# Kernel optimization log

Measured on AMD Instinct MI355X. Metric: run time of the kernel, lower is better.

## Reference

```python
import jax, jax.numpy as jnp
import numpy as np

D_MODEL = 1024
N_HEADS = 16
HEAD_DIM = D_MODEL // N_HEADS


def setup_inputs() -> dict:
    key = jax.random.key(0)
    ks = jax.random.split(key, 9)
    s = 1.0 / np.sqrt(D_MODEL)
    inp = {"x": jax.random.normal(ks[0], (4, 2048, D_MODEL), dtype=jnp.float32)}
    for i, name in enumerate(["q", "k", "v", "o"]):
        inp[f"W{name}"] = jax.random.uniform(ks[1 + i], (D_MODEL, D_MODEL), dtype=jnp.float32, minval=-s, maxval=s)
        inp[f"b{name}"] = jax.random.uniform(ks[5 + i], (D_MODEL,), dtype=jnp.float32, minval=-s, maxval=s)
    return inp


def reference(x, Wq, Wk, Wv, Wo, bq, bk, bv, bo):
    B, S, D = x.shape
    # linear layers: y = x @ W^T + b (torch nn.Linear convention)
    def proj(W, b):
        y = jnp.einsum('bsd,ed->bse', x, W) + b
        return y.reshape(B, S, N_HEADS, HEAD_DIM).transpose(0, 2, 1, 3)  # [B,H,S,hd]
    q = proj(Wq, bq)
    k = proj(Wk, bk)
    v = proj(Wv, bv)
    score = jnp.einsum('bhqd,bhkd->bhqk', q, k) / np.sqrt(HEAD_DIM)  # [B,H,S,S]
    attns = jax.nn.softmax(score, axis=-1)
    out = jnp.einsum('bhqk,bhkd->bhqd', attns, v)  # [B,H,S,hd]
    out = out.transpose(0, 2, 1, 3).reshape(B, S, D)
    return jnp.einsum('bsd,ed->bse', out, Wo) + bo
```

## Files before the change

### kernel.cpp

```cpp
#include <hip/hip_runtime.h>
#include <hip/hip_bf16.h>
#include <stdint.h>


typedef __attribute__((ext_vector_type(8))) short bfx8;
typedef __attribute__((ext_vector_type(4))) float fx4;

#define MFMA_16x16x32(A, B, C) __builtin_amdgcn_mfma_f32_16x16x32_bf16(A, B, C, 0, 0, 0)

__device__ __forceinline__ unsigned short f2bf(float f) {
  union { float f; uint32_t u; } v; v.f = f;
  uint32_t r = v.u + 0x7fffu + ((v.u >> 16) & 1u);
  return (unsigned short)(r >> 16);
}
__device__ __forceinline__ unsigned short bf16u(float f) {
  union { __hip_bfloat16 h; unsigned short u; } cv;
  cv.h = __float2bfloat16(f);
  return cv.u;
}
__device__ __forceinline__ void async16(unsigned short* l, const unsigned short* g) {
  __builtin_amdgcn_global_load_lds((const __attribute__((address_space(1))) void*)g,
                                   (__attribute__((address_space(3))) void*)l,
                                   16, 0, 0);
}

__global__ __launch_bounds__(256) void convert_f32_bf16(
    const float* __restrict__ src, unsigned short* __restrict__ dst, int n4) {
  const int i = blockIdx.x * 256 + threadIdx.x;
  if (i >= n4) return;
  const float4 v = ((const float4*)src)[i];
  ushort4 o;
  o.x = f2bf(v.x); o.y = f2bf(v.y); o.z = f2bf(v.z); o.w = f2bf(v.w);
  ((ushort4*)dst)[i] = o;
}

__global__ __launch_bounds__(256) void convert3_f32_bf16(
    const float* __restrict__ s0, const float* __restrict__ s1,
    const float* __restrict__ s2,
    unsigned short* __restrict__ d0, unsigned short* __restrict__ d1,
    unsigned short* __restrict__ d2, int n4) {
  const int which = blockIdx.y;
  const float* src = (which == 0) ? s0 : ((which == 1) ? s1 : s2);
  unsigned short* dst = (which == 0) ? d0 : ((which == 1) ? d1 : d2);
  const int i = blockIdx.x * 256 + threadIdx.x;
  if (i >= n4) return;
  const float4 v = ((const float4*)src)[i];
  ushort4 o;
  o.x = f2bf(v.x); o.y = f2bf(v.y); o.z = f2bf(v.z); o.w = f2bf(v.w);
  ((ushort4*)dst)[i] = o;
}


__global__ __launch_bounds__(256) void gemm_qkv(
    const unsigned short* __restrict__ X,
    const unsigned short* __restrict__ Wq, const unsigned short* __restrict__ Wk,
    const unsigned short* __restrict__ Wv,
    const float* __restrict__ bq, const float* __restrict__ bk,
    const float* __restrict__ bv,
    unsigned short* __restrict__ outq, unsigned short* __restrict__ outk,
    unsigned short* __restrict__ outv) {
  __shared__ unsigned short ldsA[128 * 32];
  __shared__ unsigned short ldsB[128 * 32];
  const int tid = threadIdx.x;
  const int w = tid >> 6, lane = tid & 63, quad = lane >> 4, l15 = lane & 15;
  const int m0 = blockIdx.x * 128;
  const int which = blockIdx.y >> 3;
  const int n0 = (blockIdx.y & 7) * 128;
  const unsigned short* W = (which == 0) ? Wq : ((which == 1) ? Wk : Wv);
  const float* bias       = (which == 0) ? bq : ((which == 1) ? bk : bv);
  unsigned short* Y       = (which == 0) ? outq : ((which == 1) ? outk : outv);
  const int wm = (w >> 1) * 64, wn = (w & 1) * 64;
  const int srow = tid >> 2, scol = (tid & 3) * 8;
  fx4 acc[4][4] = {};
  for (int k0 = 0; k0 < 1024; k0 += 32) {
    __syncthreads();
    async16(&ldsA[srow * 32 + scol],        X + (size_t)(m0 + srow) * 1024 + k0 + scol);
    async16(&ldsA[(srow + 64) * 32 + scol], X + (size_t)(m0 + srow + 64) * 1024 + k0 + scol);
    async16(&ldsB[srow * 32 + scol],        W + (size_t)(n0 + srow) * 1024 + k0 + scol);
    async16(&ldsB[(srow + 64) * 32 + scol], W + (size_t)(n0 + srow + 64) * 1024 + k0 + scol);
    __syncthreads();
    bfx8 af[4], bfr[4];
#pragma unroll
    for (int i = 0; i < 4; i++) af[i]  = *(const bfx8*)&ldsA[(wm + i * 16 + l15) * 32 + quad * 8];
#pragma unroll
    for (int j = 0; j < 4; j++) bfr[j] = *(const bfx8*)&ldsB[(wn + j * 16 + l15) * 32 + quad * 8];
#pragma unroll
    for (int i = 0; i < 4; i++)
#pragma unroll
      for (int j = 0; j < 4; j++)
        acc[i][j] = MFMA_16x16x32(af[i], bfr[j], acc[i][j]);
  }
  const float qscale = 0.18033688011112042f;
  float bv_[4];
#pragma unroll
  for (int j = 0; j < 4; j++) bv_[j] = bias[n0 + wn + j * 16 + l15];
#pragma unroll
  for (int i = 0; i < 4; i++) {
#pragma unroll
    for (int r = 0; r < 4; r++) {
      const int m_g = m0 + wm + i * 16 + quad * 4 + r;
      const int bb = m_g >> 11, ss = m_g & 2047;
#pragma unroll
      for (int j = 0; j < 4; j++) {
        const int n_g = n0 + wn + j * 16 + l15;
        const int h = n_g >> 6, d = n_g & 63;
        float o = acc[i][j][r] + bv_[j];
        if (which == 0) o *= qscale;
        if (which == 2)
          Y[((size_t)(bb * 16 + h) * 64 + d) * 2048 + ss] = f2bf(o);
        else
          Y[(((size_t)(bb * 16 + h)) * 2048 + ss) * 64 + d] = f2bf(o);
      }
    }
  }
}

__global__ __launch_bounds__(256) void gemm_o(
    const unsigned short* __restrict__ X,
    const unsigned short* __restrict__ W,
    const float* __restrict__ bias,
    float* __restrict__ Y) {
  __shared__ unsigned short ldsA[128 * 32];
  __shared__ unsigned short ldsB[128 * 32];
  const int tid = threadIdx.x;
  const int w = tid >> 6, lane = tid & 63, quad = lane >> 4, l15 = lane & 15;
  const int m0 = blockIdx.x * 128;
  const int n0 = blockIdx.y * 128;
  const int wm = (w >> 1) * 64, wn = (w & 1) * 64;
  const int srow = tid >> 2, scol = (tid & 3) * 8;
  fx4 acc[4][4] = {};
  for (int k0 = 0; k0 < 1024; k0 += 32) {
    __syncthreads();
    async16(&ldsA[srow * 32 + scol],        X + (size_t)(m0 + srow) * 1024 + k0 + scol);
    async16(&ldsA[(srow + 64) * 32 + scol], X + (size_t)(m0 + srow + 64) * 1024 + k0 + scol);
    async16(&ldsB[srow * 32 + scol],        W + (size_t)(n0 + srow) * 1024 + k0 + scol);
    async16(&ldsB[(srow + 64) * 32 + scol], W + (size_t)(n0 + srow + 64) * 1024 + k0 + scol);
    __syncthreads();
    bfx8 af[4], bfr[4];
#pragma unroll
    for (int i = 0; i < 4; i++) af[i]  = *(const bfx8*)&ldsA[(wm + i * 16 + l15) * 32 + quad * 8];
#pragma unroll
    for (int j = 0; j < 4; j++) bfr[j] = *(const bfx8*)&ldsB[(wn + j * 16 + l15) * 32 + quad * 8];
#pragma unroll
    for (int i = 0; i < 4; i++)
#pragma unroll
      for (int j = 0; j < 4; j++)
        acc[i][j] = MFMA_16x16x32(af[i], bfr[j], acc[i][j]);
  }
  float bv_[4];
#pragma unroll
  for (int j = 0; j < 4; j++) bv_[j] = bias[n0 + wn + j * 16 + l15];
#pragma unroll
  for (int i = 0; i < 4; i++) {
#pragma unroll
    for (int r = 0; r < 4; r++) {
      const int m_g = m0 + wm + i * 16 + quad * 4 + r;
#pragma unroll
      for (int j = 0; j < 4; j++) {
        const int n_g = n0 + wn + j * 16 + l15;
        Y[(size_t)m_g * 1024 + n_g] = acc[i][j][r] + bv_[j];
      }
    }
  }
}


#define P_LD 68

__global__ __launch_bounds__(256, 4) void attn_kernel(
    const unsigned short* __restrict__ Q, const unsigned short* __restrict__ K,
    const unsigned short* __restrict__ VT, unsigned short* __restrict__ O) {
  __shared__ unsigned short lds_k[64 * 64];
  __shared__ unsigned short lds_vt[64 * 64];
  __shared__ unsigned short lds_p[4][32 * P_LD];
  const int tid = threadIdx.x;
  const int w = tid >> 6, lane = tid & 63, quad = lane >> 4, l15 = lane & 15;
  const int bh = blockIdx.y;
  const size_t hoff = (size_t)bh * 2048 * 64;
  const unsigned short* Qh = Q + hoff;
  const unsigned short* Kh = K + hoff;
  const unsigned short* VTh = VT + hoff;
  const int q0 = blockIdx.x * 128 + w * 32;

  bfx8 qf[2][2];
#pragma unroll
  for (int s = 0; s < 2; s++) {
    qf[s][0] = *(const bfx8*)&Qh[(size_t)(q0 + s * 16 + l15) * 64 + quad * 8];
    qf[s][1] = *(const bfx8*)&Qh[(size_t)(q0 + s * 16 + l15) * 64 + 32 + quad * 8];
  }

  fx4 o_acc[2][4] = {};
  float l_r[2][4] = {};

  const int vr0 = w * 8 + (lane >> 3);
  const int vr1 = vr0 + 32;
  const int seg = lane & 7;
  const unsigned short* vsrc0 = VTh + (size_t)vr0 * 2048 + ((seg ^ (vr0 & 7)) * 8);
  const unsigned short* vsrc1 = VTh + (size_t)vr1 * 2048 + ((seg ^ (vr1 & 7)) * 8);
  unsigned short* vdst0 = &lds_vt[vr0 * 64 + seg * 8];
  unsigned short* vdst1 = &lds_vt[vr1 * 64 + seg * 8];

  const int krl = lane >> 3;
  unsigned short* kdst0 = &lds_k[(w * 16 + krl) * 64 + seg * 8];
  unsigned short* kdst1 = kdst0 + 8 * 64;
  const unsigned short* ksrc0 = Kh + (size_t)(w * 16 + krl) * 64 + ((seg ^ krl) * 8);
  const unsigned short* ksrc1 = ksrc0 + 8 * 64;

  const int s0v = (quad ^ (l15 & 7)) * 8;
  const int s1v = ((quad + 4) ^ (l15 & 7)) * 8;

  async16(kdst0, ksrc0);
  async16(kdst1, ksrc1);

  for (int t = 0; t < 32; ++t) {
    const int kv0 = t * 64;
    __syncthreads();
    async16(vdst0, vsrc0 + kv0);
    async16(vdst1, vsrc1 + kv0);

    fx4 s0a[4], s1a[4];
#pragma unroll
    for (int nj = 0; nj < 4; nj++) {
      const int krow = (nj * 16 + l15) * 64;
      bfx8 kf0 = *(const bfx8*)&lds_k[krow + s0v];
      bfx8 kf1 = *(const bfx8*)&lds_k[krow + s1v];
      fx4 z0 = {}, z1 = {};
      z0 = MFMA_16x16x32(qf[0][0], kf0, z0);
      z0 = MFMA_16x16x32(qf[0][1], kf1, z0);
      z1 = MFMA_16x16x32(qf[1][0], kf0, z1);
      z1 = MFMA_16x16x32(qf[1][1], kf1, z1);
      s0a[nj] = z0;
      s1a[nj] = z1;
    }

#pragma unroll
    for (int s = 0; s < 2; s++) {
      const fx4* sa = (s == 0) ? s0a : s1a;
#pragma unroll
      for (int r = 0; r < 4; r++) {
        float p0 = __builtin_amdgcn_exp2f(sa[0][r]);
        float p1 = __builtin_amdgcn_exp2f(sa[1][r]);
        float p2 = __builtin_amdgcn_exp2f(sa[2][r]);
        float p3 = __builtin_amdgcn_exp2f(sa[3][r]);
        l_r[s][r] += (p0 + p1) + (p2 + p3);
        const int pbase = (s * 16 + quad * 4 + r) * P_LD + l15;
        lds_p[w][pbase]      = bf16u(p0);
        lds_p[w][pbase + 16] = bf16u(p1);
        lds_p[w][pbase + 32] = bf16u(p2);
        lds_p[w][pbase + 48] = bf16u(p3);
      }
    }

    __syncthreads();

    bfx8 pf[2][2];
#pragma unroll
    for (int s = 0; s < 2; s++) {
      pf[s][0] = *(const bfx8*)&lds_p[w][(s * 16 + l15) * P_LD + quad * 8];
      pf[s][1] = *(const bfx8*)&lds_p[w][(s * 16 + l15) * P_LD + 32 + quad * 8];
    }
#pragma unroll
    for (int nj = 0; nj < 4; nj++) {
      const int vrow = (nj * 16 + l15) * 64;
      bfx8 vf0 = *(const bfx8*)&lds_vt[vrow + s0v];
      bfx8 vf1 = *(const bfx8*)&lds_vt[vrow + s1v];
      o_acc[0][nj] = MFMA_16x16x32(pf[0][0], vf0, o_acc[0][nj]);
      o_acc[0][nj] = MFMA_16x16x32(pf[0][1], vf1, o_acc[0][nj]);
      o_acc[1][nj] = MFMA_16x16x32(pf[1][0], vf0, o_acc[1][nj]);
      o_acc[1][nj] = MFMA_16x16x32(pf[1][1], vf1, o_acc[1][nj]);
    }

    if (t < 31) {
      const size_t koff = (size_t)(t + 1) * 64 * 64;
      async16(kdst0, ksrc0 + koff);
      async16(kdst1, ksrc1 + koff);
    }
  }

  const int bb = bh >> 4, h = bh & 15;
#pragma unroll
  for (int s = 0; s < 2; s++) {
#pragma unroll
    for (int r = 0; r < 4; r++) {
      float sum = l_r[s][r];
#pragma unroll
      for (int d = 1; d < 16; d <<= 1) sum += __shfl_xor(sum, d, 64);
      const float inv = 1.0f / sum;
      const int qrow = q0 + s * 16 + quad * 4 + r;
      const size_t base = ((size_t)(bb * 2048 + qrow)) * 1024 + h * 64;
#pragma unroll
      for (int nj = 0; nj < 4; nj++)
        O[base + nj * 16 + l15] = f2bf(o_acc[s][nj][r] * inv);
    }
  }
}


extern "C" void kernel_launch(void* const* d_in, const int* in_sizes, int n_in,
                              void* d_out, int out_size, void* d_ws, size_t ws_size,
                              hipStream_t stream) {
  const float* x = (const float*)d_in[0];
  const float *Wq, *Wk, *Wv, *Wo, *bq, *bk, *bv, *bo;
  if (in_sizes[2] == 1024) {
    Wq = (const float*)d_in[1]; bq = (const float*)d_in[2];
    Wk = (const float*)d_in[3]; bk = (const float*)d_in[4];
    Wv = (const float*)d_in[5]; bv = (const float*)d_in[6];
    Wo = (const float*)d_in[7]; bo = (const float*)d_in[8];
  } else {
    Wq = (const float*)d_in[1]; Wk = (const float*)d_in[2];
    Wv = (const float*)d_in[3]; Wo = (const float*)d_in[4];
    bq = (const float*)d_in[5]; bk = (const float*)d_in[6];
    bv = (const float*)d_in[7]; bo = (const float*)d_in[8];
  }
  const size_t NT = (size_t)4 * 16 * 2048 * 64;
  const size_t NW = (size_t)1024 * 1024;
  unsigned short* ws = (unsigned short*)d_ws;
  unsigned short* xb = ws;
  unsigned short* q  = ws + NT;
  unsigned short* k  = ws + 2 * NT;
  unsigned short* vt = ws + 3 * NT;
  unsigned short* ao = xb;
  unsigned short* wq = (unsigned short*)d_out;
  unsigned short* wk = wq + NW;
  unsigned short* wv = wk + NW;
  unsigned short* wo = q;

  convert_f32_bf16<<<(int)(NT / 4 + 255) / 256, 256, 0, stream>>>(x, xb, (int)(NT / 4));
  convert3_f32_bf16<<<dim3((int)(NW / 4 + 255) / 256, 3), 256, 0, stream>>>(
      Wq, Wk, Wv, wq, wk, wv, (int)(NW / 4));

  gemm_qkv<<<dim3(64, 24), 256, 0, stream>>>(xb, wq, wk, wv, bq, bk, bv, q, k, vt);
  attn_kernel<<<dim3(16, 64), 256, 0, stream>>>(q, k, vt, ao);

  convert_f32_bf16<<<(int)(NW / 4 + 255) / 256, 256, 0, stream>>>(Wo, wo, (int)(NW / 4));
  gemm_o<<<dim3(64, 8), 256, 0, stream>>>(ao, wo, bo, (float*)d_out);
}
```

Measured before the change: 298.3 us.

## Vectorize V-transpose stores and remap attention blocks to keep heads on one XCD

The QKV GEMM epilogue for the transposed V output now packs four consecutive sequence positions into one 8-byte ushort4 store, replacing four scattered 2-byte stores. The attention kernel switches to a 1D grid and decodes the block index so that all 16 query blocks of a given head land on the same XCD (blocks are dispatched round-robin across 8 XCDs). This lets that head's K/V tiles be reused from that XCD's L2. The remap assumes exactly 64 heads and 8 XCDs.

```diff
diff --git a/kernel.cpp b/kernel.cpp
--- a/kernel.cpp
+++ b/kernel.cpp
@@ -94,22 +94,38 @@
   float bv_[4];
 #pragma unroll
   for (int j = 0; j < 4; j++) bv_[j] = bias[n0 + wn + j * 16 + l15];
-#pragma unroll
-  for (int i = 0; i < 4; i++) {
-#pragma unroll
-    for (int r = 0; r < 4; r++) {
-      const int m_g = m0 + wm + i * 16 + quad * 4 + r;
+  if (which == 2) {
+#pragma unroll
+    for (int i = 0; i < 4; i++) {
+      const int m_g = m0 + wm + i * 16 + quad * 4;
       const int bb = m_g >> 11, ss = m_g & 2047;
 #pragma unroll
       for (int j = 0; j < 4; j++) {
         const int n_g = n0 + wn + j * 16 + l15;
         const int h = n_g >> 6, d = n_g & 63;
-        float o = acc[i][j][r] + bv_[j];
-        if (which == 0) o *= qscale;
-        if (which == 2)
-          Y[((size_t)(bb * 16 + h) * 64 + d) * 2048 + ss] = f2bf(o);
-        else
+        ushort4 o4;
+        o4.x = f2bf(acc[i][j][0] + bv_[j]);
+        o4.y = f2bf(acc[i][j][1] + bv_[j]);
+        o4.z = f2bf(acc[i][j][2] + bv_[j]);
+        o4.w = f2bf(acc[i][j][3] + bv_[j]);
+        *(ushort4*)&Y[((size_t)(bb * 16 + h) * 64 + d) * 2048 + ss] = o4;
+      }
+    }
+  } else {
+#pragma unroll
+    for (int i = 0; i < 4; i++) {
+#pragma unroll
+      for (int r = 0; r < 4; r++) {
+        const int m_g = m0 + wm + i * 16 + quad * 4 + r;
+        const int bb = m_g >> 11, ss = m_g & 2047;
+#pragma unroll
+        for (int j = 0; j < 4; j++) {
+          const int n_g = n0 + wn + j * 16 + l15;
+          const int h = n_g >> 6, d = n_g & 63;
+          float o = acc[i][j][r] + bv_[j];
+          if (which == 0) o *= qscale;
           Y[(((size_t)(bb * 16 + h)) * 2048 + ss) * 64 + d] = f2bf(o);
+        }
       }
     }
   }
@@ -175,12 +191,18 @@
   __shared__ unsigned short lds_p[4][32 * P_LD];
   const int tid = threadIdx.x;
   const int w = tid >> 6, lane = tid & 63, quad = lane >> 4, l15 = lane & 15;
-  const int bh = blockIdx.y;
+
+  const int lin = blockIdx.x;
+  const int xcd = lin & 7;
+  const int jj = lin >> 3;
+  const int bh = ((jj >> 4) << 3) | xcd;
+  const int qb = jj & 15;
+
   const size_t hoff = (size_t)bh * 2048 * 64;
   const unsigned short* Qh = Q + hoff;
   const unsigned short* Kh = K + hoff;
   const unsigned short* VTh = VT + hoff;
-  const int q0 = blockIdx.x * 128 + w * 32;
+  const int q0 = qb * 128 + w * 32;
 
   bfx8 qf[2][2];
 #pragma unroll
@@ -330,7 +352,7 @@
       Wq, Wk, Wv, wq, wk, wv, (int)(NW / 4));
 
   gemm_qkv<<<dim3(64, 24), 256, 0, stream>>>(xb, wq, wk, wv, bq, bk, bv, q, k, vt);
-  attn_kernel<<<dim3(16, 64), 256, 0, stream>>>(q, k, vt, ao);
+  attn_kernel<<<dim3(1024), 256, 0, stream>>>(q, k, vt, ao);
 
   convert_f32_bf16<<<(int)(NW / 4 + 255) / 256, 256, 0, stream>>>(Wo, wo, (int)(NW / 4));
   gemm_o<<<dim3(64, 8), 256, 0, stream>>>(ao, wo, bo, (float*)d_out);
```

After: 296.0 us. No clear change (-0.8%).
